# Performance work log

Hardware: AMD Instinct MI355X
Metric: run time of the kernel (lower is better)

Reference implementation:

```python
import jax, jax.numpy as jnp
import numpy as np

N_NODES = 100000
N_EDGES = 1200000
IN_CH = 64
MID_CH = 256


def setup_inputs() -> dict:
    key = jax.random.key(0)
    ks = jax.random.split(key, 10)
    x = jax.random.normal(ks[0], (N_NODES, IN_CH), dtype=jnp.float32)
    edge_index = jax.random.randint(ks[1], (2, N_EDGES), 0, N_NODES, dtype=jnp.int64)
    conv_w = jax.random.normal(ks[2], (IN_CH, IN_CH), dtype=jnp.float32) * 0.1
    conv_b = jax.random.normal(ks[3], (IN_CH,), dtype=jnp.float32) * 0.1
    w1 = jax.random.normal(ks[4], (MID_CH, IN_CH), dtype=jnp.float32) * 0.1
    b1 = jax.random.normal(ks[5], (MID_CH,), dtype=jnp.float32) * 0.1
    w2 = jax.random.normal(ks[6], (MID_CH, MID_CH), dtype=jnp.float32) * 0.05
    b2 = jax.random.normal(ks[7], (MID_CH,), dtype=jnp.float32) * 0.05
    w3 = jax.random.normal(ks[8], (1, MID_CH), dtype=jnp.float32) * 0.05
    b3 = jax.random.normal(ks[9], (1,), dtype=jnp.float32) * 0.05
    return {"x": x, "edge_index": edge_index, "conv_w": conv_w, "conv_b": conv_b,
            "w1": w1, "b1": b1, "w2": w2, "b2": b2, "w3": w3, "b3": b3}


def gcn_conv(x, src, dst, n, conv_w, conv_b):
    # PyG GCNConv: linear transform, add self-loops, symmetric normalization,
    # scatter-sum aggregation at dst, then bias.
    loop = jnp.arange(n, dtype=src.dtype)
    s = jnp.concatenate([src, loop])
    d = jnp.concatenate([dst, loop])
    h = x @ conv_w.T  # [N, C]
    deg = jax.ops.segment_sum(jnp.ones_like(d, dtype=x.dtype), d, num_segments=n)
    dinv = jax.lax.rsqrt(deg)  # self-loops guarantee deg >= 1
    norm = dinv[s] * dinv[d]  # [E+N]
    msg = h[s] * norm[:, None]  # gather + scale
    agg = jax.ops.segment_sum(msg, d, num_segments=n)  # scatter-add
    return agg + conv_b


def reference(x, edge_index, conv_w, conv_b, w1, b1, w2, b2, w3, b3):
    n = x.shape[0]
    src, dst = edge_index[0], edge_index[1]
    out = jax.nn.relu(gcn_conv(x, src, dst, n, conv_w, conv_b))
    h = out + x  # residual
    h = jax.nn.relu(h @ w1.T + b1)
    h = jax.nn.relu(h @ w2.T + b2)
    return h @ w3.T + b3  # [N, 1]
```

## Files before the change

kernel.cpp:

```cpp
#include <hip/hip_runtime.h>


typedef __bf16 bf16x8 __attribute__((ext_vector_type(8)));
typedef float f32x4 __attribute__((ext_vector_type(4)));
typedef unsigned int u32x4 __attribute__((ext_vector_type(4)));
typedef unsigned short u16x4 __attribute__((ext_vector_type(4)));

#define NSLICE 8
#define EPB 2048
#define CAP 40

__device__ inline unsigned short f2b(float f) {
    unsigned int u = __builtin_bit_cast(unsigned int, f);
    u += 0x7fff + ((u >> 16) & 1);
    return (unsigned short)(u >> 16);
}

__device__ inline bf16x8 ld_frag16(const void* p) {
    u32x4 v = *(const u32x4*)p;
    return __builtin_bit_cast(bf16x8, v);
}

__global__ __launch_bounds__(256) void k_gemm1z(const float* __restrict__ x,
                                                const float* __restrict__ cw,
                                                int* __restrict__ cnt,
                                                unsigned short* __restrict__ h2, int N) {
    __shared__ float xt[64][64];
    int t = threadIdx.x;
    int gi = blockIdx.x * 256 + t;
    if (gi < N) cnt[gi] = 0;

    int lane = t & 63;
    int wv = t >> 6;
    int n0 = blockIdx.x * 64;

    float4 w[16];
    const float4* cw4 = (const float4*)(cw + lane * 64);
    #pragma unroll
    for (int i = 0; i < 16; i++) w[i] = cw4[i];

    const float4* x4 = (const float4*)x;
    float4* xt4 = (float4*)(&xt[0][0]);
    #pragma unroll
    for (int i = 0; i < 4; i++) {
        int idx = t + i * 256;
        int row = idx >> 4;
        int node = n0 + row;
        xt4[idx] = (node < N) ? x4[(size_t)node * 16 + (idx & 15)]
                              : make_float4(0.f, 0.f, 0.f, 0.f);
    }
    __syncthreads();

    for (int nl = wv * 16; nl < wv * 16 + 16; ++nl) {
        int node = n0 + nl;
        if (node >= N) break;
        const float4* xr = (const float4*)(&xt[nl][0]);
        float a = 0.f;
        #pragma unroll
        for (int i = 0; i < 16; i++) {
            float4 xv = xr[i];
            a += w[i].x * xv.x; a += w[i].y * xv.y;
            a += w[i].z * xv.z; a += w[i].w * xv.w;
        }
        h2[(size_t)node * 64 + lane] = f2b(a);
    }
}

__global__ void k_fill(const int* __restrict__ src, const int* __restrict__ dst, int E,
                       int* __restrict__ cnt, int* __restrict__ csrf,
                       const float* __restrict__ w1, const float* __restrict__ w2,
                       unsigned short* __restrict__ w1b, unsigned short* __restrict__ w2b,
                       int sliceSz) {
    int bid = blockIdx.x;
    int t = threadIdx.x;
    if (bid < 256) {
        int i = bid * 256 + t;
        if (i < 16384) w1b[i] = f2b(w1[i]);
        w2b[i] = f2b(w2[i]);
    }
    int slice = bid & (NSLICE - 1);
    int chunk = bid >> 3;
    int lo = slice * sliceSz, hi = lo + sliceSz;
    int base = chunk * EPB;
    #pragma unroll
    for (int it = 0; it < EPB / 256; it++) {
        int i = base + it * 256 + t;
        if (i < E) {
            int d = dst[i];
            if (d >= lo && d < hi) {
                int pos = atomicAdd(&cnt[d], 1);
                if (pos < CAP) csrf[(size_t)d * CAP + pos] = src[i];
            }
        }
    }
}

__global__ __launch_bounds__(256) void k_agg(const unsigned short* __restrict__ h2,
                                             const int* __restrict__ csrf,
                                             const int* __restrict__ cnt,
                                             const float* __restrict__ cb,
                                             const float* __restrict__ x,
                                             unsigned short* __restrict__ hres, int N) {
    int t = threadIdx.x;
    int lane = t & 63;
    int wv = t >> 6;
    int d = blockIdx.x * 4 + wv;
    if (d >= N) return;
    int degTrue = cnt[d];
    float dinvd = rsqrtf((float)(degTrue + 1));
    int deg = degTrue > CAP ? CAP : degTrue;
    int half = lane >> 5;
    int ch = lane & 31;
    int cvec = d;
    if (lane < deg) cvec = csrf[(size_t)d * CAP + lane];
    float dlv = rsqrtf((float)(cnt[cvec] + 1));

    const unsigned int* h2u = (const unsigned int*)h2;
    unsigned int sv = h2u[(size_t)d * 32 + ch];
    float a0 = 0.f, a1 = 0.f;
    if (half == 0) {
        a0 += dinvd * __builtin_bit_cast(float, (sv & 0xffffu) << 16);
        a1 += dinvd * __builtin_bit_cast(float, sv & 0xffff0000u);
    }
    for (int j = 0; j < deg; j += 16) {
        #pragma unroll
        for (int p = 0; p < 8; p++) {
            int e = j + 2 * p + half;
            int s = __shfl(cvec, e);
            float ds = __shfl(dlv, e);
            unsigned int v = h2u[(size_t)s * 32 + ch];
            v = (e < deg) ? v : 0u;
            a0 += ds * __builtin_bit_cast(float, (v & 0xffffu) << 16);
            a1 += ds * __builtin_bit_cast(float, v & 0xffff0000u);
        }
    }
    a0 += __shfl_xor(a0, 32);
    a1 += __shfl_xor(a1, 32);
    float2 cbv = ((const float2*)cb)[ch];
    float2 xv = ((const float2*)x)[(size_t)d * 32 + ch];
    float o0 = fmaxf(a0 * dinvd + cbv.x, 0.f) + xv.x;
    float o1 = fmaxf(a1 * dinvd + cbv.y, 0.f) + xv.y;
    if (half == 0) {
        unsigned int o = (unsigned int)f2b(o0) | ((unsigned int)f2b(o1) << 16);
        ((unsigned int*)hres)[(size_t)d * 32 + ch] = o;
    }
}

__global__ __launch_bounds__(512, 4) void k_mlp(const unsigned short* __restrict__ hres,
                                                const unsigned short* __restrict__ w1b,
                                                const float* __restrict__ b1,
                                                const unsigned short* __restrict__ w2b,
                                                const float* __restrict__ b2,
                                                const float* __restrict__ w3,
                                                const float* __restrict__ b3,
                                                float* __restrict__ out, int N) {
    __shared__ unsigned short h1t[32768];
    __shared__ unsigned short ht[8192];
    char* h1b = (char*)h1t;
    char* htb = (char*)ht;

    int t = threadIdx.x;
    int lane = t & 63;
    int wid = t >> 6;
    int wm = wid >> 2;
    int wn = wid & 3;
    int lr = lane & 15;
    int lk = (lane >> 4) * 8;
    int lg = lane >> 4;
    int n0 = blockIdx.x * 128;

    {
        const u16x4* hr4 = (const u16x4*)hres;
        #pragma unroll
        for (int i = 0; i < 4; i++) {
            int idx = t + i * 512;
            int row = idx >> 4;
            int c4 = idx & 15;
            int node = n0 + row;
            u16x4 v = {0, 0, 0, 0};
            if (node < N) v = hr4[(size_t)node * 16 + c4];
            int byte = (row << 7) + (c4 << 3);
            byte ^= (row & 7) << 4;
            *(u16x4*)(htb + byte) = v;
        }
    }
    __syncthreads();

    float bias1[4];
    #pragma unroll
    for (int nf = 0; nf < 4; nf++) bias1[nf] = b1[wn * 64 + nf * 16 + lr];

    f32x4 acc[4][4];
    #pragma unroll
    for (int mf = 0; mf < 4; mf++)
        #pragma unroll
        for (int nf = 0; nf < 4; nf++) {
            acc[mf][nf][0] = bias1[nf]; acc[mf][nf][1] = bias1[nf];
            acc[mf][nf][2] = bias1[nf]; acc[mf][nf][3] = bias1[nf];
        }

    #pragma unroll
    for (int kk = 0; kk < 2; kk++) {
        bf16x8 af[4], bfg[4];
        #pragma unroll
        for (int mf = 0; mf < 4; mf++) {
            int row = wm * 64 + mf * 16 + lr;
            int byte = (row << 7) + ((kk * 32 + lk) << 1);
            byte ^= (row & 7) << 4;
            af[mf] = ld_frag16(htb + byte);
        }
        #pragma unroll
        for (int nf = 0; nf < 4; nf++) {
            int c = wn * 64 + nf * 16 + lr;
            bfg[nf] = ld_frag16(w1b + c * 64 + kk * 32 + lk);
        }
        #pragma unroll
        for (int mf = 0; mf < 4; mf++)
            #pragma unroll
            for (int nf = 0; nf < 4; nf++)
                acc[mf][nf] = __builtin_amdgcn_mfma_f32_16x16x32_bf16(af[mf], bfg[nf], acc[mf][nf], 0, 0, 0);
    }

    #pragma unroll
    for (int mf = 0; mf < 4; mf++)
        #pragma unroll
        for (int nf = 0; nf < 4; nf++)
            #pragma unroll
            for (int r = 0; r < 4; r++) {
                int row = wm * 64 + mf * 16 + lg * 4 + r;
                int col = wn * 64 + nf * 16 + lr;
                float v = fmaxf(acc[mf][nf][r], 0.f);
                int byte = (row << 9) + (col << 1);
                byte ^= (row & 7) << 4;
                *(unsigned short*)(h1b + byte) = f2b(v);
            }
    __syncthreads();

    float bias2[4];
    #pragma unroll
    for (int nf = 0; nf < 4; nf++) bias2[nf] = b2[wn * 64 + nf * 16 + lr];
    #pragma unroll
    for (int mf = 0; mf < 4; mf++)
        #pragma unroll
        for (int nf = 0; nf < 4; nf++) {
            acc[mf][nf][0] = bias2[nf]; acc[mf][nf][1] = bias2[nf];
            acc[mf][nf][2] = bias2[nf]; acc[mf][nf][3] = bias2[nf];
        }

    #pragma unroll
    for (int kk = 0; kk < 8; kk++) {
        bf16x8 af[4], bfg[4];
        #pragma unroll
        for (int nf = 0; nf < 4; nf++) {
            int j = wn * 64 + nf * 16 + lr;
            bfg[nf] = ld_frag16(w2b + j * 256 + kk * 32 + lk);
        }
        #pragma unroll
        for (int mf = 0; mf < 4; mf++) {
            int row = wm * 64 + mf * 16 + lr;
            int byte = (row << 9) + ((kk * 32 + lk) << 1);
            byte ^= (row & 7) << 4;
            af[mf] = ld_frag16(h1b + byte);
        }
        #pragma unroll
        for (int mf = 0; mf < 4; mf++)
            #pragma unroll
            for (int nf = 0; nf < 4; nf++)
                acc[mf][nf] = __builtin_amdgcn_mfma_f32_16x16x32_bf16(af[mf], bfg[nf], acc[mf][nf], 0, 0, 0);
    }

    float w3v[4];
    #pragma unroll
    for (int nf = 0; nf < 4; nf++) w3v[nf] = w3[wn * 64 + nf * 16 + lr];

    float* red = (float*)htb;
    __syncthreads();

    #pragma unroll
    for (int mf = 0; mf < 4; mf++)
        #pragma unroll
        for (int r = 0; r < 4; r++) {
            float p = 0.f;
            #pragma unroll
            for (int nf = 0; nf < 4; nf++)
                p += fmaxf(acc[mf][nf][r], 0.f) * w3v[nf];
            p += __shfl_xor(p, 1);
            p += __shfl_xor(p, 2);
            p += __shfl_xor(p, 4);
            p += __shfl_xor(p, 8);
            if (lr == 0) {
                int row = wm * 64 + mf * 16 + lg * 4 + r;
                red[wn * 128 + row] = p;
            }
        }
    __syncthreads();

    if (t < 128) {
        int node = n0 + t;
        if (node < N) {
            float s = b3[0] + red[t] + red[128 + t] + red[256 + t] + red[384 + t];
            out[node] = s;
        }
    }
}

extern "C" void kernel_launch(void* const* d_in, const int* in_sizes, int n_in,
                              void* d_out, int out_size, void* d_ws, size_t ws_size,
                              hipStream_t stream) {
    const float* x  = (const float*)d_in[0];
    const int*   ei = (const int*)d_in[1];
    const float* cw = (const float*)d_in[2];
    const float* cb = (const float*)d_in[3];
    const float* w1 = (const float*)d_in[4];
    const float* b1 = (const float*)d_in[5];
    const float* w2 = (const float*)d_in[6];
    const float* b2 = (const float*)d_in[7];
    const float* w3 = (const float*)d_in[8];
    const float* b3 = (const float*)d_in[9];
    float* out = (float*)d_out;

    int N = in_sizes[0] / 64;
    int E = in_sizes[1] / 2;
    const int* src = ei;
    const int* dst = ei + E;

    char* ws = (char*)d_ws;
    size_t off = 0;
    auto alloc = [&](size_t bytes) {
        off = (off + 255) & ~(size_t)255;
        char* p = ws + off;
        off += bytes;
        return p;
    };
    int*            cnt   = (int*)alloc((size_t)N * 4);
    int*            csrf  = (int*)alloc((size_t)N * CAP * 4);
    unsigned short* h2    = (unsigned short*)alloc((size_t)N * 64 * 2);
    unsigned short* hresb = (unsigned short*)alloc((size_t)N * 64 * 2);
    unsigned short* w1b   = (unsigned short*)alloc((size_t)16384 * 2);
    unsigned short* w2b   = (unsigned short*)alloc((size_t)65536 * 2);
    (void)ws_size; (void)n_in; (void)out_size;

    k_gemm1z<<<(N + 63) / 64, 256, 0, stream>>>(x, cw, cnt, h2, N);

    int sliceSz = (N + NSLICE - 1) / NSLICE;
    int chunks = (E + EPB - 1) / EPB;
    k_fill<<<chunks * NSLICE, 256, 0, stream>>>(src, dst, E, cnt, csrf,
                                                w1, w2, w1b, w2b, sliceSz);

    k_agg<<<(N + 3) / 4, 256, 0, stream>>>(h2, csrf, cnt, cb, x, hresb, N);

    k_mlp<<<(N + 127) / 128, 512, 0, stream>>>(hresb, w1b, b1, w2b, b2, w3, b3, out, N);
}
```

Baseline: 271.3 us.

## Widen aggregation gathers to 8-byte loads and tune CSR fill

The aggregation kernel now has 16 lanes cover a 64-channel row with uint2 loads, so four edges are processed per wave step instead of two. Loop iterations past the remaining degree are skipped, and the partial sums are reduced with two xor shuffles. The fill kernel uses nontemporal loads, reads src only when the destination falls in its slice, and uses a smaller edges-per-block constant, which launches more blocks. The weight-to-bf16 conversion moves from the fill kernel into the first GEMM kernel, taking that work off the atomic-heavy fill path.

```diff
diff --git a/kernel.cpp b/kernel.cpp
--- a/kernel.cpp
+++ b/kernel.cpp
@@ -7,7 +7,7 @@
 typedef unsigned short u16x4 __attribute__((ext_vector_type(4)));
 
 #define NSLICE 8
-#define EPB 2048
+#define EPB 1024
 #define CAP 40
 
 __device__ inline unsigned short f2b(float f) {
@@ -16,6 +16,13 @@
     return (unsigned short)(u >> 16);
 }
 
+__device__ inline float blo(unsigned int v) {
+    return __builtin_bit_cast(float, (v & 0xffffu) << 16);
+}
+__device__ inline float bhi(unsigned int v) {
+    return __builtin_bit_cast(float, v & 0xffff0000u);
+}
+
 __device__ inline bf16x8 ld_frag16(const void* p) {
     u32x4 v = *(const u32x4*)p;
     return __builtin_bit_cast(bf16x8, v);
@@ -23,12 +30,20 @@
 
 __global__ __launch_bounds__(256) void k_gemm1z(const float* __restrict__ x,
                                                 const float* __restrict__ cw,
+                                                const float* __restrict__ w1,
+                                                const float* __restrict__ w2,
+                                                unsigned short* __restrict__ w1b,
+                                                unsigned short* __restrict__ w2b,
                                                 int* __restrict__ cnt,
                                                 unsigned short* __restrict__ h2, int N) {
     __shared__ float xt[64][64];
     int t = threadIdx.x;
     int gi = blockIdx.x * 256 + t;
     if (gi < N) cnt[gi] = 0;
+    if (gi < 65536) {
+        if (gi < 16384) w1b[gi] = f2b(w1[gi]);
+        w2b[gi] = f2b(w2[gi]);
+    }
 
     int lane = t & 63;
     int wv = t >> 6;
@@ -67,17 +82,9 @@
 }
 
 __global__ void k_fill(const int* __restrict__ src, const int* __restrict__ dst, int E,
-                       int* __restrict__ cnt, int* __restrict__ csrf,
-                       const float* __restrict__ w1, const float* __restrict__ w2,
-                       unsigned short* __restrict__ w1b, unsigned short* __restrict__ w2b,
-                       int sliceSz) {
+                       int* __restrict__ cnt, int* __restrict__ csrf, int sliceSz) {
     int bid = blockIdx.x;
     int t = threadIdx.x;
-    if (bid < 256) {
-        int i = bid * 256 + t;
-        if (i < 16384) w1b[i] = f2b(w1[i]);
-        w2b[i] = f2b(w2[i]);
-    }
     int slice = bid & (NSLICE - 1);
     int chunk = bid >> 3;
     int lo = slice * sliceSz, hi = lo + sliceSz;
@@ -86,10 +93,11 @@
     for (int it = 0; it < EPB / 256; it++) {
         int i = base + it * 256 + t;
         if (i < E) {
-            int d = dst[i];
+            int d = __builtin_nontemporal_load(&dst[i]);
             if (d >= lo && d < hi) {
+                int s = __builtin_nontemporal_load(&src[i]);
                 int pos = atomicAdd(&cnt[d], 1);
-                if (pos < CAP) csrf[(size_t)d * CAP + pos] = src[i];
+                if (pos < CAP) csrf[(size_t)d * CAP + pos] = s;
             }
         }
     }
@@ -109,40 +117,49 @@
     int degTrue = cnt[d];
     float dinvd = rsqrtf((float)(degTrue + 1));
     int deg = degTrue > CAP ? CAP : degTrue;
-    int half = lane >> 5;
-    int ch = lane & 31;
+    int cq = lane & 15;
+    int e4 = lane >> 4;
     int cvec = d;
-    if (lane < deg) cvec = csrf[(size_t)d * CAP + lane];
+    if (lane < deg) cvec = __builtin_nontemporal_load(&csrf[(size_t)d * CAP + lane]);
     float dlv = rsqrtf((float)(cnt[cvec] + 1));
 
-    const unsigned int* h2u = (const unsigned int*)h2;
-    unsigned int sv = h2u[(size_t)d * 32 + ch];
-    float a0 = 0.f, a1 = 0.f;
-    if (half == 0) {
-        a0 += dinvd * __builtin_bit_cast(float, (sv & 0xffffu) << 16);
-        a1 += dinvd * __builtin_bit_cast(float, sv & 0xffff0000u);
-    }
-    for (int j = 0; j < deg; j += 16) {
+    const uint2* h2v = (const uint2*)h2;
+    float a0 = 0.f, a1 = 0.f, a2 = 0.f, a3 = 0.f;
+    if (e4 == 0) {
+        uint2 sv = h2v[(size_t)d * 16 + cq];
+        a0 = dinvd * blo(sv.x); a1 = dinvd * bhi(sv.x);
+        a2 = dinvd * blo(sv.y); a3 = dinvd * bhi(sv.y);
+    }
+    for (int j = 0; j < deg; j += 32) {
+        int rem = deg - j;
         #pragma unroll
         for (int p = 0; p < 8; p++) {
-            int e = j + 2 * p + half;
-            int s = __shfl(cvec, e);
-            float ds = __shfl(dlv, e);
-            unsigned int v = h2u[(size_t)s * 32 + ch];
-            v = (e < deg) ? v : 0u;
-            a0 += ds * __builtin_bit_cast(float, (v & 0xffffu) << 16);
-            a1 += ds * __builtin_bit_cast(float, v & 0xffff0000u);
-        }
-    }
-    a0 += __shfl_xor(a0, 32);
-    a1 += __shfl_xor(a1, 32);
-    float2 cbv = ((const float2*)cb)[ch];
-    float2 xv = ((const float2*)x)[(size_t)d * 32 + ch];
-    float o0 = fmaxf(a0 * dinvd + cbv.x, 0.f) + xv.x;
-    float o1 = fmaxf(a1 * dinvd + cbv.y, 0.f) + xv.y;
-    if (half == 0) {
-        unsigned int o = (unsigned int)f2b(o0) | ((unsigned int)f2b(o1) << 16);
-        ((unsigned int*)hres)[(size_t)d * 32 + ch] = o;
+            if (p * 4 < rem) {
+                int e = j + p * 4 + e4;
+                int s = __shfl(cvec, e);
+                float ds = __shfl(dlv, e);
+                uint2 v = h2v[(size_t)s * 16 + cq];
+                float m = (e < deg) ? ds : 0.f;
+                a0 += m * blo(v.x); a1 += m * bhi(v.x);
+                a2 += m * blo(v.y); a3 += m * bhi(v.y);
+            }
+        }
+    }
+    a0 += __shfl_xor(a0, 16); a0 += __shfl_xor(a0, 32);
+    a1 += __shfl_xor(a1, 16); a1 += __shfl_xor(a1, 32);
+    a2 += __shfl_xor(a2, 16); a2 += __shfl_xor(a2, 32);
+    a3 += __shfl_xor(a3, 16); a3 += __shfl_xor(a3, 32);
+    if (e4 == 0) {
+        float4 cbv = ((const float4*)cb)[cq];
+        float4 xv = ((const float4*)x)[(size_t)d * 16 + cq];
+        float o0 = fmaxf(a0 * dinvd + cbv.x, 0.f) + xv.x;
+        float o1 = fmaxf(a1 * dinvd + cbv.y, 0.f) + xv.y;
+        float o2 = fmaxf(a2 * dinvd + cbv.z, 0.f) + xv.z;
+        float o3 = fmaxf(a3 * dinvd + cbv.w, 0.f) + xv.w;
+        uint2 o;
+        o.x = (unsigned int)f2b(o0) | ((unsigned int)f2b(o1) << 16);
+        o.y = (unsigned int)f2b(o2) | ((unsigned int)f2b(o3) << 16);
+        ((uint2*)hres)[(size_t)d * 16 + cq] = o;
     }
 }
 
@@ -340,12 +357,11 @@
     unsigned short* w2b   = (unsigned short*)alloc((size_t)65536 * 2);
     (void)ws_size; (void)n_in; (void)out_size;
 
-    k_gemm1z<<<(N + 63) / 64, 256, 0, stream>>>(x, cw, cnt, h2, N);
+    k_gemm1z<<<(N + 63) / 64, 256, 0, stream>>>(x, cw, w1, w2, w1b, w2b, cnt, h2, N);
 
     int sliceSz = (N + NSLICE - 1) / NSLICE;
     int chunks = (E + EPB - 1) / EPB;
-    k_fill<<<chunks * NSLICE, 256, 0, stream>>>(src, dst, E, cnt, csrf,
-                                                w1, w2, w1b, w2b, sliceSz);
+    k_fill<<<chunks * NSLICE, 256, 0, stream>>>(src, dst, E, cnt, csrf, sliceSz);
 
     k_agg<<<(N + 3) / 4, 256, 0, stream>>>(h2, csrf, cnt, cb, x, hresb, N);
 
```

Measured after the change: 291.7 us. 1.07x slower.
